# Kernel optimization log

Measured on AMD Instinct MI355X. Metric: run time of the kernel, lower is better.

## Reference

```python
import jax, jax.numpy as jnp
import numpy as np

H_HEADS = 16
D_K = 64
D_V = 64
D_MODEL = H_HEADS * D_K  # 1024
B, S = 2, 2048


def _xavier(key, shape):
    fan_in, fan_out = shape
    limit = float(np.sqrt(6.0 / (fan_in + fan_out)))
    return jax.random.uniform(key, shape, jnp.float32, -limit, limit)


def setup_inputs() -> dict:
    key = jax.random.key(0)
    ks = jax.random.split(key, 6)
    return {
        "batch": jax.random.normal(ks[0], (B, S, D_MODEL), jnp.float32),
        "attention_mask": jnp.zeros((S, S), jnp.float32),
        "W_Q": _xavier(ks[1], (D_MODEL, H_HEADS * D_K)),
        "W_K": _xavier(ks[2], (D_MODEL, H_HEADS * D_K)),
        "W_V": _xavier(ks[3], (D_MODEL, H_HEADS * D_V)),
        "b_Q": jnp.zeros((H_HEADS * D_K,), jnp.float32),
        "b_K": jnp.zeros((H_HEADS * D_K,), jnp.float32),
        "b_V": jnp.zeros((H_HEADS * D_V,), jnp.float32),
        "W_O": _xavier(ks[4], (H_HEADS * D_V, D_MODEL)),
        "b_O": jnp.zeros((D_MODEL,), jnp.float32),
    }


def reference(batch, attention_mask, W_Q, W_K, W_V, b_Q, b_K, b_V, W_O, b_O):
    # Batched equivalent of the per-head loop: project all heads at once,
    # then split the last dim into (h, d). Same math, one GEMM each.
    q = batch @ W_Q + b_Q  # [B,S,h*dk]
    k = batch @ W_K + b_K
    v = batch @ W_V + b_V
    q = q.reshape(B, S, H_HEADS, D_K)
    k = k.reshape(B, S, H_HEADS, D_K)
    v = v.reshape(B, S, H_HEADS, D_V)
    scale = 1.0 / jnp.sqrt(jnp.asarray(D_K, jnp.float32))
    scores = jnp.einsum("bqhd,bkhd->bhqk", q, k) * scale  # [B,h,S,S]
    scores = scores + attention_mask  # broadcast over batch & heads
    attn = jax.nn.softmax(scores, axis=-1)
    out = jnp.einsum("bhqk,bkhd->bqhd", attn, v)  # [B,S,h,dv]
    out = out.reshape(B, S, H_HEADS * D_V)  # concat over heads
    return out @ W_O + b_O
```

## Files before the change

kernel.cpp:

```cpp
#include <hip/hip_runtime.h>
#include <hip/hip_bf16.h>

typedef __attribute__((ext_vector_type(8))) short bf16x8;
typedef __attribute__((ext_vector_type(4))) float f32x4;
typedef __attribute__((ext_vector_type(4))) unsigned short u16x4;
typedef __attribute__((ext_vector_type(8))) unsigned short u16x8;

#define DEVI static __device__ __forceinline__

DEVI unsigned short f2bf(float f) {
  union { __hip_bfloat16 h; unsigned short u; } cv;
  cv.h = __float2bfloat16(f);
  return cv.u;
}

DEVI float bf2f(unsigned short u) {
  union { unsigned int i; float f; } cv;
  cv.i = (unsigned int)u << 16;
  return cv.f;
}

DEVI void gld_lds16(const unsigned short* g, unsigned short* l) {
  __builtin_amdgcn_global_load_lds(
      (const __attribute__((address_space(1))) unsigned int*)g,
      (__attribute__((address_space(3))) unsigned int*)l, 16, 0, 0);
}

__global__ void k_prep(const float* __restrict__ batch, const float* __restrict__ mask,
                       const float* __restrict__ Wq, const float* __restrict__ Wk,
                       const float* __restrict__ Wv, const float* __restrict__ Wo,
                       const float* __restrict__ bq, const float* __restrict__ bk,
                       const float* __restrict__ bv,
                       unsigned short* __restrict__ xb, unsigned short* __restrict__ wqkvT,
                       unsigned short* __restrict__ woT, unsigned short* __restrict__ mU,
                       float* __restrict__ bcat) {
  __shared__ float lt[32][33];
  int bid = blockIdx.x, tid = threadIdx.x;
  if (bid < 4096) {
    int i = bid * 256 + tid;
    f32x4 v = *((const f32x4*)batch + i);
    u16x4 o;
#pragma unroll
    for (int j = 0; j < 4; ++j) o[j] = f2bf(v[j]);
    *((u16x4*)xb + i) = o;
  } else if (bid < 8192) {
    int t = bid - 4096;
    int g = t >> 10, r = t & 1023, kt = r >> 5, nt = r & 31;
    const float* W = (g == 0) ? Wq : (g == 1) ? Wk : (g == 2) ? Wv : Wo;
    unsigned short* out = (g < 3) ? (wqkvT + (size_t)g * 1024 * 1024) : woT;
    int row = tid >> 3, c4 = tid & 7;
    f32x4 v = *(const f32x4*)(W + (size_t)(kt * 32 + row) * 1024 + nt * 32 + c4 * 4);
#pragma unroll
    for (int j = 0; j < 4; ++j) lt[row][c4 * 4 + j] = v[j];
    __syncthreads();
    u16x4 o;
#pragma unroll
    for (int j = 0; j < 4; ++j) o[j] = f2bf(lt[c4 * 4 + j][row]);
    *(u16x4*)(out + (size_t)(nt * 32 + row) * 1024 + kt * 32 + c4 * 4) = o;
  } else if (bid < 12288) {
    int r = bid - 8192;
    int k0 = (r & 63) * 32, q0 = (r >> 6) * 32;
    int row = tid >> 3, c4 = tid & 7;
    f32x4 v = *(const f32x4*)(mask + (size_t)(q0 + row) * 2048 + k0 + c4 * 4);
#pragma unroll
    for (int j = 0; j < 4; ++j) lt[row][c4 * 4 + j] = v[j] * 1.4426950408889634f;
    __syncthreads();
    int kq = tid >> 5, qr = tid & 31;
    u16x4 o;
#pragma unroll
    for (int j = 0; j < 4; ++j) o[j] = f2bf(lt[qr][kq * 4 + j]);
    *(u16x4*)(mU + ((size_t)(k0 >> 2) + kq) * 8192 + (size_t)(q0 + qr) * 4) = o;
  } else {
    int i = (bid - 12288) * 256 + tid;
    if (i < 3072) bcat[i] = (i < 1024) ? bq[i] : (i < 2048) ? bk[i - 1024] : bv[i - 2048];
  }
}

template <int OUT_MODE, int BM, int BN, int NT>
__launch_bounds__(256)
__global__ void k_gemm(const unsigned short* __restrict__ A,
                       const unsigned short* __restrict__ Bt,
                       const float* __restrict__ bias,
                       void* __restrict__ C0, void* __restrict__ C1,
                       void* __restrict__ C2, int K) {
  constexpr int MF = BM / 32, NF = BN / 32, CA = BM / 32, CB = BN / 32;
  __shared__ unsigned short lA[BM * 64];
  __shared__ unsigned short lB[BN * 64];
  int tid = threadIdx.x;
  int fid = blockIdx.x;
  int nwg8 = gridDim.x >> 3;
  int swz = (fid & 7) * nwg8 + (fid >> 3);
  int n0 = (swz % NT) * BN, m0 = (swz / NT) * BM;
  int w = tid >> 6, l = tid & 63;
  int wm = (w >> 1) * (BM / 2), wn = (w & 1) * (BN / 2);
  int lg = l >> 4, lc = l & 15;
  f32x4 acc[MF][NF] = {};
  const unsigned short* Ab = A + (size_t)m0 * K;
  const unsigned short* Bb = Bt + (size_t)n0 * K;

  for (int kk = 0; kk < K; kk += 64) {
#pragma unroll
    for (int i = 0; i < CA; ++i) {
      int c = tid + i * 256;
      gld_lds16(Ab + (size_t)(c >> 3) * K + kk + (c & 7) * 8, lA + c * 8);
    }
#pragma unroll
    for (int i = 0; i < CB; ++i) {
      int c = tid + i * 256;
      gld_lds16(Bb + (size_t)(c >> 3) * K + kk + (c & 7) * 8, lB + c * 8);
    }
    __syncthreads();
#pragma unroll
    for (int ks = 0; ks < 2; ++ks) {
      bf16x8 af[MF], bfr[NF];
#pragma unroll
      for (int mf = 0; mf < MF; ++mf)
        af[mf] = *(const bf16x8*)(lA + (wm + mf * 16 + lc) * 64 + ks * 32 + lg * 8);
#pragma unroll
      for (int nf = 0; nf < NF; ++nf)
        bfr[nf] = *(const bf16x8*)(lB + (wn + nf * 16 + lc) * 64 + ks * 32 + lg * 8);
#pragma unroll
      for (int mf = 0; mf < MF; ++mf)
#pragma unroll
        for (int nf = 0; nf < NF; ++nf)
          acc[mf][nf] = __builtin_amdgcn_mfma_f32_16x16x32_bf16(af[mf], bfr[nf], acc[mf][nf], 0, 0, 0);
    }
    __syncthreads();
  }

  float bv[NF];
#pragma unroll
  for (int nf = 0; nf < NF; ++nf) bv[nf] = bias[n0 + wn + nf * 16 + lc];

  if (OUT_MODE == 0) {
#pragma unroll
    for (int mf = 0; mf < MF; ++mf)
#pragma unroll
      for (int nf = 0; nf < NF; ++nf)
#pragma unroll
        for (int rr = 0; rr < 4; ++rr) {
          size_t gm = m0 + wm + mf * 16 + lg * 4 + rr;
          size_t gn = n0 + wn + nf * 16 + lc;
          ((float*)C0)[gm * (NT * BN) + gn] = acc[mf][nf][rr] + bv[nf];
        }
  } else {
    if (n0 >= 2048) {
      int bB = m0 >> 11;
      int sB = m0 & 2047;
#pragma unroll
      for (int p = 0; p < 2; ++p) {
        if ((w & 1) == p) {
#pragma unroll
          for (int mf = 0; mf < MF; ++mf)
#pragma unroll
            for (int nf = 0; nf < NF; ++nf) {
              int dl = nf * 16 + lc;
              int q0w = wm + mf * 16 + lg * 4;
              u16x4 pk;
#pragma unroll
              for (int rr = 0; rr < 4; ++rr) pk[rr] = f2bf(acc[mf][nf][rr] + bv[nf]);
              *(u16x4*)(lA + dl * 128 + (q0w ^ ((dl & 15) << 3))) = pk;
            }
        }
        __syncthreads();
        int r = tid >> 2, seg = tid & 3;
        size_t vrow = ((size_t)bB * 1024 + (n0 - 2048) + p * 64 + r) * 2048 + sB;
#pragma unroll
        for (int k = 0; k < 4; ++k) {
          u16x8 ov = *(const u16x8*)(lA + r * 128 + ((seg * 32 + k * 8) ^ ((r & 15) << 3)));
          *(u16x8*)((unsigned short*)C2 + vrow + seg * 32 + k * 8) = ov;
        }
        __syncthreads();
      }
    } else {
      int tensor = (n0 + wn) >> 10;
      unsigned short* dst = tensor ? (unsigned short*)C1 : (unsigned short*)C0;
      int goff = tensor << 10;
#pragma unroll
      for (int mf = 0; mf < MF; ++mf)
#pragma unroll
        for (int nf = 0; nf < NF; ++nf)
#pragma unroll
          for (int rr = 0; rr < 4; ++rr) {
            size_t gm = m0 + wm + mf * 16 + lg * 4 + rr;
            size_t gn = n0 + wn + nf * 16 + lc;
            dst[gm * 1024 + (gn - goff)] = f2bf(acc[mf][nf][rr] + bv[nf]);
          }
    }
  }
}

__launch_bounds__(256, 4)
__global__ void k_attn(const unsigned short* __restrict__ Qo,
                       const unsigned short* __restrict__ Ko,
                       const unsigned short* __restrict__ Vt,
                       const unsigned short* __restrict__ mU,
                       unsigned short* __restrict__ ao) {
  __shared__ unsigned short lK[2][64 * 64];
  __shared__ unsigned short lV[2][64 * 64];
  __shared__ unsigned short lP[64 * 64];
  int wg0 = blockIdx.x;
  int wg = (wg0 & 7) * 128 + (wg0 >> 3);
  int b = wg >> 9, r0 = wg & 511, h = r0 >> 5, qt = r0 & 31;
  int tid = threadIdx.x, w = tid >> 6, l = tid & 63;
  int lg = l >> 4, lc = l & 15, cb = lc & 7;
  int q0 = qt * 64 + w * 16;

  const unsigned short* Qb = Qo + (size_t)(b * 2048 + q0) * 1024 + h * 64;
  const unsigned short* Kb = Ko + (size_t)(b * 2048) * 1024 + h * 64;
  const unsigned short* Vb = Vt + (size_t)(b * 1024 + h * 64) * 2048;
  const unsigned short* mUb = mU + (size_t)lg * 8192 + (size_t)(q0 + lc) * 4;
  unsigned short* lPw = lP + (w * 16 + lc) * 64;

  int rsub = l >> 3, scol = ((l & 7) ^ rsub) * 8;

  bf16x8 qf[2];
#pragma unroll
  for (int ks = 0; ks < 2; ++ks)
    qf[ks] = *(const bf16x8*)(Qb + (size_t)lc * 1024 + ks * 32 + lg * 8);

  f32x4 o2[4] = {};
  float ll = 0.f;

#pragma unroll
  for (int i = 0; i < 2; ++i) {
    int r = i * 32 + w * 8 + rsub;
    gld_lds16(Kb + (size_t)r * 1024 + scol, &lK[0][(i * 4 + w) * 512]);
    gld_lds16(Vb + (size_t)r * 2048 + scol, &lV[0][(i * 4 + w) * 512]);
  }
  __syncthreads();

  int cur = 0;
  for (int t = 0; t < 32; ++t) {
    int k0 = t * 64;
    if (t < 31) {
#pragma unroll
      for (int i = 0; i < 2; ++i) {
        int r = i * 32 + w * 8 + rsub;
        gld_lds16(Kb + (size_t)(k0 + 64 + r) * 1024 + scol, &lK[cur ^ 1][(i * 4 + w) * 512]);
        gld_lds16(Vb + (size_t)r * 2048 + k0 + 64 + scol, &lV[cur ^ 1][(i * 4 + w) * 512]);
      }
    }
    u16x4 mv[4];
#pragma unroll
    for (int blk = 0; blk < 4; ++blk)
      mv[blk] = *(const u16x4*)(mUb + ((size_t)t * 16 + blk * 4) * 8192);

    const unsigned short* lKc = lK[cur];
    const unsigned short* lVc = lV[cur];

    f32x4 s[4] = {};
    __builtin_amdgcn_s_setprio(1);
#pragma unroll
    for (int ks = 0; ks < 2; ++ks) {
      bf16x8 kf[4];
#pragma unroll
      for (int blk = 0; blk < 4; ++blk)
        kf[blk] = *(const bf16x8*)(lKc + (blk * 16 + lc) * 64 +
                                   ((ks * 32 + lg * 8) ^ (cb << 3)));
#pragma unroll
      for (int blk = 0; blk < 4; ++blk)
        s[blk] = __builtin_amdgcn_mfma_f32_16x16x32_bf16(kf[blk], qf[ks], s[blk], 0, 0, 0);
    }
    __builtin_amdgcn_s_setprio(0);

    float psum = 0.f;
#pragma unroll
    for (int blk = 0; blk < 4; ++blk) {
      u16x4 pk;
#pragma unroll
      for (int rr = 0; rr < 4; ++rr) {
        float p = exp2f(fmaf(s[blk][rr], 0.18033688011112042f, bf2f(mv[blk][rr])));
        psum += p;
        pk[rr] = f2bf(p);
      }
      *(u16x4*)(lPw + (((blk * 32 + lg * 8) ^ (cb << 4)) >> 1)) = pk;
    }
    ll += psum;

#pragma unroll
    for (int ks2 = 0; ks2 < 2; ++ks2) {
      bf16x8 pa = *(const bf16x8*)(lPw + (((ks2 * 64 + lg * 16) ^ (cb << 4)) >> 1));
      bf16x8 vf[4];
#pragma unroll
      for (int nf = 0; nf < 4; ++nf)
        vf[nf] = *(const bf16x8*)(lVc + (nf * 16 + lc) * 64 +
                                  ((ks2 * 32 + lg * 8) ^ (cb << 3)));
      __builtin_amdgcn_s_setprio(1);
#pragma unroll
      for (int nf = 0; nf < 4; ++nf)
        o2[nf] = __builtin_amdgcn_mfma_f32_16x16x32_bf16(vf[nf], pa, o2[nf], 0, 0, 0);
      __builtin_amdgcn_s_setprio(0);
    }

    __syncthreads();
    cur ^= 1;
  }

  ll += __shfl_xor(ll, 16);
  ll += __shfl_xor(ll, 32);
  float inv = 1.f / ll;
#pragma unroll
  for (int nf = 0; nf < 4; ++nf) {
    u16x4 pk;
#pragma unroll
    for (int rr = 0; rr < 4; ++rr) pk[rr] = f2bf(o2[nf][rr] * inv);
    *(u16x4*)(lPw + (((nf * 32 + lg * 8) ^ (cb << 4)) >> 1)) = pk;
  }
  int rq = l >> 2, seg = l & 3, c2 = rq & 7;
  const unsigned short* lPr = lP + (w * 16 + rq) * 64;
#pragma unroll
  for (int half = 0; half < 2; ++half) {
    u16x8 ov = *(const u16x8*)(lPr + (((seg * 32 + half * 16) ^ (c2 << 4)) >> 1));
    *(u16x8*)(ao + (size_t)(b * 2048 + q0 + rq) * 1024 + h * 64 + seg * 16 + half * 8) = ov;
  }
}

extern "C" void kernel_launch(void* const* d_in, const int* in_sizes, int n_in,
                              void* d_out, int out_size, void* d_ws, size_t ws_size,
                              hipStream_t stream) {
  const float* batch = (const float*)d_in[0];
  const float* mask = (const float*)d_in[1];
  const float* Wq = (const float*)d_in[2];
  const float* Wk = (const float*)d_in[3];
  const float* Wv = (const float*)d_in[4];
  const float* bq = (const float*)d_in[5];
  const float* bk = (const float*)d_in[6];
  const float* bvv = (const float*)d_in[7];
  const float* Wo = (const float*)d_in[8];
  const float* bo = (const float*)d_in[9];

  char* ws = (char*)d_ws;
  unsigned short* Xb    = (unsigned short*)(ws);
  unsigned short* WqkvT = (unsigned short*)(ws + 8388608);
  unsigned short* WoT   = (unsigned short*)(ws + 14680064);
  float*          bcat  = (float*)(ws + 16777216);
  unsigned short* Qo    = (unsigned short*)(ws + 16789504);
  unsigned short* Ko    = (unsigned short*)(ws + 25178112);
  unsigned short* Vt    = (unsigned short*)(ws + 33566720);
  unsigned short* AO    = (unsigned short*)(ws + 41955328);
  unsigned short* mU    = (unsigned short*)(ws + 50343936);

  hipLaunchKernelGGL(k_prep, dim3(12300), dim3(256), 0, stream,
                     batch, mask, Wq, Wk, Wv, Wo, bq, bk, bvv,
                     Xb, WqkvT, WoT, mU, bcat);
  hipLaunchKernelGGL((k_gemm<1, 128, 128, 24>), dim3(768), dim3(256), 0, stream,
                     Xb, WqkvT, bcat, (void*)Qo, (void*)Ko, (void*)Vt, 1024);
  hipLaunchKernelGGL(k_attn, dim3(1024), dim3(256), 0, stream, Qo, Ko, Vt, mU, AO);
  hipLaunchKernelGGL((k_gemm<0, 128, 64, 16>), dim3(512), dim3(256), 0, stream,
                     AO, WoT, bo, (void*)d_out, nullptr, nullptr, 1024);
}
```

Measured before the change: 248.1 us.

## Double-buffer GEMM K-loop with 32-wide tiles and pack softmax math into float2

The projection GEMM kernel now loads 32-wide K slices into two LDS buffers, prefetching the next slice while MFMAs run on the current one. This replaces the single 64-wide buffer that stalled on every load, and it halves LDS use per buffer at the cost of twice as many loop iterations and barriers. In the attention kernel, the softmax scale-add and the row-sum accumulation are rewritten with float2 vectors so the compiler can emit packed FP32 ops.

```diff
diff --git a/kernel.cpp b/kernel.cpp
--- a/kernel.cpp
+++ b/kernel.cpp
@@ -3,6 +3,7 @@
 
 typedef __attribute__((ext_vector_type(8))) short bf16x8;
 typedef __attribute__((ext_vector_type(4))) float f32x4;
+typedef __attribute__((ext_vector_type(2))) float f32x2;
 typedef __attribute__((ext_vector_type(4))) unsigned short u16x4;
 typedef __attribute__((ext_vector_type(8))) unsigned short u16x8;
 
@@ -83,9 +84,10 @@
                        const float* __restrict__ bias,
                        void* __restrict__ C0, void* __restrict__ C1,
                        void* __restrict__ C2, int K) {
-  constexpr int MF = BM / 32, NF = BN / 32, CA = BM / 32, CB = BN / 32;
-  __shared__ unsigned short lA[BM * 64];
-  __shared__ unsigned short lB[BN * 64];
+  constexpr int MFw = BM / 32, NFw = BN / 32;
+  constexpr int CA = BM / 64, CB = BN / 64;
+  __shared__ unsigned short lA[2][BM * 32];
+  __shared__ unsigned short lB[2][BN * 32];
   int tid = threadIdx.x;
   int fid = blockIdx.x;
   int nwg8 = gridDim.x >> 3;
@@ -94,49 +96,63 @@
   int w = tid >> 6, l = tid & 63;
   int wm = (w >> 1) * (BM / 2), wn = (w & 1) * (BN / 2);
   int lg = l >> 4, lc = l & 15;
-  f32x4 acc[MF][NF] = {};
+  f32x4 acc[MFw][NFw] = {};
   const unsigned short* Ab = A + (size_t)m0 * K;
   const unsigned short* Bb = Bt + (size_t)n0 * K;
-
-  for (int kk = 0; kk < K; kk += 64) {
-#pragma unroll
-    for (int i = 0; i < CA; ++i) {
-      int c = tid + i * 256;
-      gld_lds16(Ab + (size_t)(c >> 3) * K + kk + (c & 7) * 8, lA + c * 8);
-    }
-#pragma unroll
-    for (int i = 0; i < CB; ++i) {
-      int c = tid + i * 256;
-      gld_lds16(Bb + (size_t)(c >> 3) * K + kk + (c & 7) * 8, lB + c * 8);
-    }
+  int NK = K >> 5;
+
+#pragma unroll
+  for (int i = 0; i < CA; ++i) {
+    int c = tid + i * 256;
+    gld_lds16(Ab + (size_t)(c >> 2) * K + (c & 3) * 8, &lA[0][c * 8]);
+  }
+#pragma unroll
+  for (int i = 0; i < CB; ++i) {
+    int c = tid + i * 256;
+    gld_lds16(Bb + (size_t)(c >> 2) * K + (c & 3) * 8, &lB[0][c * 8]);
+  }
+  __syncthreads();
+
+  int cur = 0;
+  for (int kt = 0; kt < NK; ++kt) {
+    if (kt + 1 < NK) {
+      int kk = (kt + 1) << 5;
+#pragma unroll
+      for (int i = 0; i < CA; ++i) {
+        int c = tid + i * 256;
+        gld_lds16(Ab + (size_t)(c >> 2) * K + kk + (c & 3) * 8, &lA[cur ^ 1][c * 8]);
+      }
+#pragma unroll
+      for (int i = 0; i < CB; ++i) {
+        int c = tid + i * 256;
+        gld_lds16(Bb + (size_t)(c >> 2) * K + kk + (c & 3) * 8, &lB[cur ^ 1][c * 8]);
+      }
+    }
+    bf16x8 af[MFw], bfr[NFw];
+#pragma unroll
+    for (int mf = 0; mf < MFw; ++mf)
+      af[mf] = *(const bf16x8*)(&lA[cur][(wm + mf * 16 + lc) * 32 + lg * 8]);
+#pragma unroll
+    for (int nf = 0; nf < NFw; ++nf)
+      bfr[nf] = *(const bf16x8*)(&lB[cur][(wn + nf * 16 + lc) * 32 + lg * 8]);
+#pragma unroll
+    for (int mf = 0; mf < MFw; ++mf)
+#pragma unroll
+      for (int nf = 0; nf < NFw; ++nf)
+        acc[mf][nf] = __builtin_amdgcn_mfma_f32_16x16x32_bf16(af[mf], bfr[nf], acc[mf][nf], 0, 0, 0);
     __syncthreads();
-#pragma unroll
-    for (int ks = 0; ks < 2; ++ks) {
-      bf16x8 af[MF], bfr[NF];
-#pragma unroll
-      for (int mf = 0; mf < MF; ++mf)
-        af[mf] = *(const bf16x8*)(lA + (wm + mf * 16 + lc) * 64 + ks * 32 + lg * 8);
-#pragma unroll
-      for (int nf = 0; nf < NF; ++nf)
-        bfr[nf] = *(const bf16x8*)(lB + (wn + nf * 16 + lc) * 64 + ks * 32 + lg * 8);
-#pragma unroll
-      for (int mf = 0; mf < MF; ++mf)
-#pragma unroll
-        for (int nf = 0; nf < NF; ++nf)
-          acc[mf][nf] = __builtin_amdgcn_mfma_f32_16x16x32_bf16(af[mf], bfr[nf], acc[mf][nf], 0, 0, 0);
-    }
-    __syncthreads();
-  }
-
-  float bv[NF];
-#pragma unroll
-  for (int nf = 0; nf < NF; ++nf) bv[nf] = bias[n0 + wn + nf * 16 + lc];
+    cur ^= 1;
+  }
+
+  float bv[NFw];
+#pragma unroll
+  for (int nf = 0; nf < NFw; ++nf) bv[nf] = bias[n0 + wn + nf * 16 + lc];
 
   if (OUT_MODE == 0) {
 #pragma unroll
-    for (int mf = 0; mf < MF; ++mf)
-#pragma unroll
-      for (int nf = 0; nf < NF; ++nf)
+    for (int mf = 0; mf < MFw; ++mf)
+#pragma unroll
+      for (int nf = 0; nf < NFw; ++nf)
 #pragma unroll
         for (int rr = 0; rr < 4; ++rr) {
           size_t gm = m0 + wm + mf * 16 + lg * 4 + rr;
@@ -144,6 +160,7 @@
           ((float*)C0)[gm * (NT * BN) + gn] = acc[mf][nf][rr] + bv[nf];
         }
   } else {
+    unsigned short* lAf = &lA[0][0];
     if (n0 >= 2048) {
       int bB = m0 >> 11;
       int sB = m0 & 2047;
@@ -151,15 +168,15 @@
       for (int p = 0; p < 2; ++p) {
         if ((w & 1) == p) {
 #pragma unroll
-          for (int mf = 0; mf < MF; ++mf)
-#pragma unroll
-            for (int nf = 0; nf < NF; ++nf) {
+          for (int mf = 0; mf < MFw; ++mf)
+#pragma unroll
+            for (int nf = 0; nf < NFw; ++nf) {
               int dl = nf * 16 + lc;
               int q0w = wm + mf * 16 + lg * 4;
               u16x4 pk;
 #pragma unroll
               for (int rr = 0; rr < 4; ++rr) pk[rr] = f2bf(acc[mf][nf][rr] + bv[nf]);
-              *(u16x4*)(lA + dl * 128 + (q0w ^ ((dl & 15) << 3))) = pk;
+              *(u16x4*)(lAf + dl * 128 + (q0w ^ ((dl & 15) << 3))) = pk;
             }
         }
         __syncthreads();
@@ -167,7 +184,7 @@
         size_t vrow = ((size_t)bB * 1024 + (n0 - 2048) + p * 64 + r) * 2048 + sB;
 #pragma unroll
         for (int k = 0; k < 4; ++k) {
-          u16x8 ov = *(const u16x8*)(lA + r * 128 + ((seg * 32 + k * 8) ^ ((r & 15) << 3)));
+          u16x8 ov = *(const u16x8*)(lAf + r * 128 + ((seg * 32 + k * 8) ^ ((r & 15) << 3)));
           *(u16x8*)((unsigned short*)C2 + vrow + seg * 32 + k * 8) = ov;
         }
         __syncthreads();
@@ -177,9 +194,9 @@
       unsigned short* dst = tensor ? (unsigned short*)C1 : (unsigned short*)C0;
       int goff = tensor << 10;
 #pragma unroll
-      for (int mf = 0; mf < MF; ++mf)
-#pragma unroll
-        for (int nf = 0; nf < NF; ++nf)
+      for (int mf = 0; mf < MFw; ++mf)
+#pragma unroll
+        for (int nf = 0; nf < NFw; ++nf)
 #pragma unroll
           for (int rr = 0; rr < 4; ++rr) {
             size_t gm = m0 + wm + mf * 16 + lg * 4 + rr;
@@ -220,7 +237,7 @@
     qf[ks] = *(const bf16x8*)(Qb + (size_t)lc * 1024 + ks * 32 + lg * 8);
 
   f32x4 o2[4] = {};
-  float ll = 0.f;
+  f32x2 ll2 = {0.f, 0.f};
 
 #pragma unroll
   for (int i = 0; i < 2; ++i) {
@@ -264,19 +281,23 @@
     }
     __builtin_amdgcn_s_setprio(0);
 
-    float psum = 0.f;
 #pragma unroll
     for (int blk = 0; blk < 4; ++blk) {
       u16x4 pk;
 #pragma unroll
-      for (int rr = 0; rr < 4; ++rr) {
-        float p = exp2f(fmaf(s[blk][rr], 0.18033688011112042f, bf2f(mv[blk][rr])));
-        psum += p;
-        pk[rr] = f2bf(p);
+      for (int rp = 0; rp < 2; ++rp) {
+        f32x2 sv2, mk2;
+        sv2[0] = s[blk][2 * rp];     sv2[1] = s[blk][2 * rp + 1];
+        mk2[0] = bf2f(mv[blk][2 * rp]); mk2[1] = bf2f(mv[blk][2 * rp + 1]);
+        f32x2 lg2 = sv2 * 0.18033688011112042f + mk2;
+        float p0 = exp2f(lg2[0]), p1 = exp2f(lg2[1]);
+        f32x2 p2; p2[0] = p0; p2[1] = p1;
+        ll2 += p2;
+        pk[2 * rp] = f2bf(p0);
+        pk[2 * rp + 1] = f2bf(p1);
       }
       *(u16x4*)(lPw + (((blk * 32 + lg * 8) ^ (cb << 4)) >> 1)) = pk;
     }
-    ll += psum;
 
 #pragma unroll
     for (int ks2 = 0; ks2 < 2; ++ks2) {
@@ -297,6 +318,7 @@
     cur ^= 1;
   }
 
+  float ll = ll2[0] + ll2[1];
   ll += __shfl_xor(ll, 16);
   ll += __shfl_xor(ll, 32);
   float inv = 1.f / ll;
```

After: 230.0 us. -7.3%, faster.
